# Kernel optimization log

Measured on AMD Instinct MI355X. Metric: run time of the kernel, lower is better.

Reference implementation:

```python
import jax, jax.numpy as jnp
import numpy as np

N_HEAD = 8
LINEAR_DIM = 64
IN_PIXELS = 4096  # h*w = 64*64
D = N_HEAD * LINEAR_DIM  # 512
C = 128
LN_EPS = 1e-6
BN_EPS = 1e-5


def setup_inputs() -> dict:
    key = jax.random.key(0)
    ks = jax.random.split(key, 10)
    shp = (16, C, 64, 64)
    # Kaiming-uniform-ish small init for weights (torch Linear weight layout: [out, in])
    def lin(k, out_f, in_f):
        lim = 1.0 / np.sqrt(in_f)
        return jax.random.uniform(k, (out_f, in_f), jnp.float32, -lim, lim)
    return {
        "v": jax.random.normal(ks[0], shp, jnp.float32),
        "k": jax.random.normal(ks[1], shp, jnp.float32),
        "q": jax.random.normal(ks[2], shp, jnp.float32),
        "w_qs": lin(ks[3], D, IN_PIXELS),
        "w_ks": lin(ks[4], D, IN_PIXELS),
        "w_vs": lin(ks[5], D, IN_PIXELS),
        "w_fc": lin(ks[6], IN_PIXELS, D),
        "ln_gamma": jnp.ones((D,), jnp.float32),
        "ln_beta": jnp.zeros((D,), jnp.float32),
        "temperature": jnp.asarray(IN_PIXELS ** 0.5, jnp.float32),
        "bn_gamma": jnp.ones((C,), jnp.float32),
        "bn_beta": jnp.zeros((C,), jnp.float32),
    }


def _layer_norm(x, gamma, beta):
    # torch-faithful: unbiased std (ddof=1), divide by (std + eps)
    mean = jnp.mean(x, axis=-1, keepdims=True)
    var = jnp.var(x, axis=-1, keepdims=True, ddof=1)
    std = jnp.sqrt(var)
    return gamma * (x - mean) / (std + LN_EPS) + beta


def reference(v, k, q, w_qs, w_ks, w_vs, w_fc, ln_gamma, ln_beta, temperature, bn_gamma, bn_beta):
    b, c, h, w = q.shape
    P = h * w
    qf = q.reshape(b, c, P)
    kf = k.reshape(b, c, P)
    vf = v.reshape(b, c, P)
    residual = vf
    # QKV projections: [b,c,P] @ W^T -> [b,c,D] -> [b,nh,c,ld]
    def proj(x, W):
        y = jnp.einsum('bcp,dp->bcd', x, W)
        return y.reshape(b, c, N_HEAD, LINEAR_DIM).transpose(0, 2, 1, 3)
    Q = proj(qf, w_qs)
    K = proj(kf, w_ks)
    V = proj(vf, w_vs)
    # channel-wise attention: scores [b,nh,c,c]
    scores = jnp.einsum('bhcd,bhed->bhce', Q / temperature, K)
    attn = jax.nn.softmax(scores, axis=-1)
    O = jnp.einsum('bhce,bhed->bhcd', attn, V)
    O = O.transpose(0, 2, 1, 3).reshape(b, c, N_HEAD * LINEAR_DIM)
    # Swish -> LayerNorm -> fc -> residual
    O = O * jax.nn.sigmoid(O)
    O = _layer_norm(O, ln_gamma, ln_beta)
    O = jnp.einsum('bcd,pd->bcp', O, w_fc)
    out = (residual + O).reshape(b, c, h, w)
    # BatchNorm2d in training mode: batch stats over (b,h,w), biased variance
    mean = jnp.mean(out, axis=(0, 2, 3), keepdims=True)
    var = jnp.var(out, axis=(0, 2, 3), keepdims=True)
    out = (out - mean) / jnp.sqrt(var + BN_EPS)
    out = out * bn_gamma[None, :, None, None] + bn_beta[None, :, None, None]
    return out
```

## Files before the change

### kernel.cpp

```cpp
#include <hip/hip_runtime.h>
#include <hip/hip_bf16.h>
#include <stdint.h>

typedef __attribute__((ext_vector_type(8))) short bf16x8;
typedef __attribute__((ext_vector_type(4))) float f32x4;

#define AS1(p) ((const __attribute__((address_space(1))) uint32_t*)(p))
#define AS3(p) ((__attribute__((address_space(3))) uint32_t*)(p))

__device__ __forceinline__ ushort f2bf(float f) {
  uint32_t u = __float_as_uint(f);
  uint32_t r = (u + 0x7fffu + ((u >> 16) & 1u)) >> 16;
  return (ushort)r;
}

__device__ __forceinline__ float bf2f(ushort u) {
  uint32_t v = ((uint32_t)u) << 16;
  return __uint_as_float(v);
}

__device__ __forceinline__ uint4 cvt8u(float4 a0, float4 a1) {
  uint4 r;
  asm("v_cvt_pk_bf16_f32 %0, %1, %2" : "=v"(r.x) : "v"(a0.x), "v"(a0.y));
  asm("v_cvt_pk_bf16_f32 %0, %1, %2" : "=v"(r.y) : "v"(a0.z), "v"(a0.w));
  asm("v_cvt_pk_bf16_f32 %0, %1, %2" : "=v"(r.z) : "v"(a1.x), "v"(a1.y));
  asm("v_cvt_pk_bf16_f32 %0, %1, %2" : "=v"(r.w) : "v"(a1.z), "v"(a1.w));
  return r;
}

__global__ __launch_bounds__(256) void pack4(
    const float* __restrict__ s0, const float* __restrict__ s1,
    const float* __restrict__ s2, const float* __restrict__ s3,
    ushort* __restrict__ o0, ushort* __restrict__ o1,
    ushort* __restrict__ o2, ushort* __restrict__ o3, int n)
{
  const float* s; ushort* o;
  switch (blockIdx.y) {
    case 0: s = s0; o = o0; break;
    case 1: s = s1; o = o1; break;
    case 2: s = s2; o = o2; break;
    default: s = s3; o = o3; break;
  }
  int stride = gridDim.x * 1024;
  for (int i = (blockIdx.x * 256 + threadIdx.x) * 4; i < n; i += stride) {
    float4 v = *(const float4*)(s + i);
    ushort4 u;
    u.x = f2bf(v.x); u.y = f2bf(v.y); u.z = f2bf(v.z); u.w = f2bf(v.w);
    *(ushort4*)(o + i) = u;
  }
}

__global__ __launch_bounds__(256) void gemm_qkv(
    const float* __restrict__ aq, const float* __restrict__ ak, const float* __restrict__ av,
    const ushort* __restrict__ wq, const ushort* __restrict__ wk, const ushort* __restrict__ wv,
    ushort* __restrict__ part, int lgs)
{
  __shared__ __align__(16) ushort At[128 * 64];
  __shared__ __align__(16) ushort Bt[2][128 * 64];
  int per = gridDim.x >> 3;
  int bid = blockIdx.x;
  int swz = (bid & 7) * per + (bid >> 3);
  int y = swz & 3, x = (swz >> 2) & 15, zz = swz >> 6;
  int g = zz >> lgs, s = zz & ((1 << lgs) - 1);
  const float* A; const ushort* Bm;
  if (g == 0)      { A = aq; Bm = wq; }
  else if (g == 1) { A = ak; Bm = wk; }
  else             { A = av; Bm = wv; }
  ushort* Pd = part + ((size_t)zz) * 1048576;
  const int K = 4096;
  const int kchunk = K >> lgs;
  const int k0 = s * kchunk, kend = k0 + kchunk;
  int rowBase = x * 128;
  int colBase = y * 128;
  int tid = threadIdx.x, l = tid & 63, w = tid >> 6;
  int wr = w >> 1, wc = w & 1, fr = l & 15, fq = l >> 4;

  int arow = tid >> 3;
  int aslot = tid & 7;
  const float* Abase = A + (size_t)(rowBase + arow) * K + aslot * 8;

  f32x4 acc[4][4];
#pragma unroll
  for (int m = 0; m < 4; ++m)
#pragma unroll
    for (int n = 0; n < 4; ++n) acc[m][n] = (f32x4){0.f, 0.f, 0.f, 0.f};

  float4 areg[4][2];
  auto loadA = [&](int ktn) {
#pragma unroll
    for (int j = 0; j < 4; ++j) {
      const float* p = Abase + (size_t)(j * 32) * K + ktn;
      areg[j][0] = *(const float4*)p;
      areg[j][1] = *(const float4*)(p + 4);
    }
  };
  auto cvtWriteA = [&]() {
#pragma unroll
    for (int j = 0; j < 4; ++j) {
      int row = j * 32 + arow;
      int sw = aslot ^ (row & 7);
      *(uint4*)((char*)At + row * 128 + sw * 16) = cvt8u(areg[j][0], areg[j][1]);
    }
  };
  auto stageB = [&](ushort* Bbuf, int ktn) {
#pragma unroll
    for (int j = 0; j < 4; ++j) {
      int c = ((w * 4 + j) << 6) + l;
      int row = c >> 3, slot = c & 7;
      int srccol = (slot ^ (row & 7)) * 8;
      __builtin_amdgcn_global_load_lds(AS1(Bm + (size_t)(colBase + row) * K + ktn + srccol),
                                       AS3((char*)Bbuf + c * 16), 16, 0, 0);
    }
  };
  auto mfmaPhase = [&](const ushort* Bbuf) {
#pragma unroll
    for (int kc = 0; kc < 2; ++kc) {
      bf16x8 af[4], bv[4];
#pragma unroll
      for (int m = 0; m < 4; ++m) {
        int r = wr * 64 + m * 16 + fr;
        int sl = (kc * 4 + fq) ^ (fr & 7);
        af[m] = *(const bf16x8*)((const char*)At + r * 128 + sl * 16);
      }
#pragma unroll
      for (int n = 0; n < 4; ++n) {
        int r = wc * 64 + n * 16 + fr;
        int sl = (kc * 4 + fq) ^ (fr & 7);
        bv[n] = *(const bf16x8*)((const char*)Bbuf + r * 128 + sl * 16);
      }
#pragma unroll
      for (int m = 0; m < 4; ++m)
#pragma unroll
        for (int n = 0; n < 4; ++n)
          acc[m][n] = __builtin_amdgcn_mfma_f32_16x16x32_bf16(af[m], bv[n], acc[m][n], 0, 0, 0);
    }
  };

  loadA(k0);
  stageB(Bt[0], k0);
  cvtWriteA();
  __syncthreads();

  int buf = 0;
#pragma unroll 1
  for (int kt = k0; kt < kend; kt += 64) {
    bool more = (kt + 64) < kend;
    if (more) { loadA(kt + 64); stageB(Bt[buf ^ 1], kt + 64); }
    mfmaPhase(Bt[buf]);
    __syncthreads();
    if (more) cvtWriteA();
    __syncthreads();
    buf ^= 1;
  }

#pragma unroll
  for (int m = 0; m < 4; ++m)
#pragma unroll
    for (int n = 0; n < 4; ++n)
#pragma unroll
      for (int r = 0; r < 4; ++r) {
        int row = rowBase + wr * 64 + m * 16 + fq * 4 + r;
        int col = colBase + wc * 64 + n * 16 + fr;
        Pd[(size_t)row * 512 + col] = f2bf(acc[m][n][r]);
      }
}

__global__ __launch_bounds__(256) void reduce_qkv(
    const ushort* __restrict__ part, ushort* __restrict__ Qp, ushort* __restrict__ Kp,
    ushort* __restrict__ Vp, int lgs)
{
  int g = blockIdx.y;
  ushort* dst = g == 0 ? Qp : (g == 1 ? Kp : Vp);
  const ushort* p = part + (((size_t)g) << lgs) * 1048576;
  int i = (blockIdx.x * 256 + threadIdx.x) * 8;
  int splits = 1 << lgs;
  float accv[8];
  {
    bf16x8 v = *(const bf16x8*)(p + i);
#pragma unroll
    for (int j = 0; j < 8; ++j) accv[j] = bf2f((ushort)v[j]);
  }
  for (int s = 1; s < splits; ++s) {
    bf16x8 v = *(const bf16x8*)(p + (size_t)s * 1048576 + i);
#pragma unroll
    for (int j = 0; j < 8; ++j) accv[j] += bf2f((ushort)v[j]);
  }
  ushort u[8];
#pragma unroll
  for (int j = 0; j < 8; ++j) u[j] = f2bf(accv[j]);
  *(uint4*)(dst + i) = *(uint4*)u;
}

__global__ __launch_bounds__(256) void attn(
    const ushort* __restrict__ Qp, const ushort* __restrict__ Kp, const ushort* __restrict__ Vp,
    float* __restrict__ Obuf, const float* __restrict__ temp)
{
  __shared__ __align__(16) ushort Qs[64 * 64];
  __shared__ __align__(16) ushort Ks[128 * 64];
  __shared__ __align__(16) ushort Vt[64 * 128];
  __shared__ __align__(16) float  Sl[64 * 128];
  __shared__ __align__(16) ushort Pl[64 * 128];
  __shared__ float rsum[64];
  int bh = blockIdx.y, b = bh >> 3, h = bh & 7;
  int c0 = blockIdx.x * 64;
  int tid = threadIdx.x, l = tid & 63, w = tid >> 6;
  int wr = w >> 1, wc = w & 1, fr = l & 15, fq = l >> 4;
  float invT = 1.0f / temp[0];
  const size_t rowQ = (size_t)(b * 128 + c0);

#pragma unroll
  for (int j = 0; j < 2; ++j) {
    int c = ((w * 2 + j) << 6) + l, row = c >> 3, cc = c & 7;
    __builtin_amdgcn_global_load_lds(AS1(Qp + (rowQ + row) * 512 + h * 64 + cc * 8),
                                     AS3((char*)Qs + (w * 2 + j) * 1024), 16, 0, 0);
  }
#pragma unroll
  for (int j = 0; j < 4; ++j) {
    int c = ((w * 4 + j) << 6) + l, row = c >> 3, cc = c & 7;
    __builtin_amdgcn_global_load_lds(AS1(Kp + (size_t)(b * 128 + row) * 512 + h * 64 + cc * 8),
                                     AS3((char*)Ks + (w * 4 + j) * 1024), 16, 0, 0);
  }
#pragma unroll
  for (int t = 0; t < 4; ++t) {
    int ch = tid + t * 256, e = ch >> 3, d0 = (ch & 7) * 8;
    bf16x8 vv = *(const bf16x8*)(Vp + (size_t)(b * 128 + e) * 512 + h * 64 + d0);
#pragma unroll
    for (int j = 0; j < 8; ++j) Vt[(d0 + j) * 128 + e] = (ushort)vv[j];
  }
  __syncthreads();

  f32x4 sa[2][4];
#pragma unroll
  for (int m = 0; m < 2; ++m)
#pragma unroll
    for (int n = 0; n < 4; ++n) sa[m][n] = (f32x4){0.f, 0.f, 0.f, 0.f};
#pragma unroll
  for (int kc = 0; kc < 2; ++kc) {
    bf16x8 aQ[2], bK[4];
#pragma unroll
    for (int m = 0; m < 2; ++m)
      aQ[m] = *(const bf16x8*)&Qs[(wr * 32 + m * 16 + fr) * 64 + kc * 32 + fq * 8];
#pragma unroll
    for (int n = 0; n < 4; ++n)
      bK[n] = *(const bf16x8*)&Ks[(wc * 64 + n * 16 + fr) * 64 + kc * 32 + fq * 8];
#pragma unroll
    for (int m = 0; m < 2; ++m)
#pragma unroll
      for (int n = 0; n < 4; ++n)
        sa[m][n] = __builtin_amdgcn_mfma_f32_16x16x32_bf16(aQ[m], bK[n], sa[m][n], 0, 0, 0);
  }
#pragma unroll
  for (int m = 0; m < 2; ++m)
#pragma unroll
    for (int n = 0; n < 4; ++n)
#pragma unroll
      for (int r = 0; r < 4; ++r)
        Sl[(wr * 32 + m * 16 + fq * 4 + r) * 128 + wc * 64 + n * 16 + fr] = sa[m][n][r] * invT;
  __syncthreads();

  {
    int row = tid >> 2, qq = tid & 3;
    const float* srow = Sl + row * 128 + qq * 32;
    float4 va[8];
#pragma unroll
    for (int i = 0; i < 8; ++i) va[i] = *(const float4*)(srow + i * 4);
    float mx = -1e30f;
#pragma unroll
    for (int i = 0; i < 8; ++i)
      mx = fmaxf(mx, fmaxf(fmaxf(va[i].x, va[i].y), fmaxf(va[i].z, va[i].w)));
    mx = fmaxf(mx, __shfl_xor(mx, 1));
    mx = fmaxf(mx, __shfl_xor(mx, 2));
    float ssum = 0.f;
    ushort* prow = Pl + row * 128 + qq * 32;
#pragma unroll
    for (int i = 0; i < 8; ++i) {
      float e0 = __expf(va[i].x - mx), e1 = __expf(va[i].y - mx);
      float e2 = __expf(va[i].z - mx), e3 = __expf(va[i].w - mx);
      ssum += (e0 + e1) + (e2 + e3);
      ushort4 u; u.x = f2bf(e0); u.y = f2bf(e1); u.z = f2bf(e2); u.w = f2bf(e3);
      *(ushort4*)(prow + i * 4) = u;
    }
    ssum += __shfl_xor(ssum, 1);
    ssum += __shfl_xor(ssum, 2);
    if (qq == 0) rsum[row] = ssum;
  }
  __syncthreads();

  f32x4 oa[2][2];
#pragma unroll
  for (int m = 0; m < 2; ++m)
#pragma unroll
    for (int n = 0; n < 2; ++n) oa[m][n] = (f32x4){0.f, 0.f, 0.f, 0.f};
#pragma unroll
  for (int kc = 0; kc < 4; ++kc) {
    bf16x8 aP[2], bV[2];
#pragma unroll
    for (int m = 0; m < 2; ++m)
      aP[m] = *(const bf16x8*)&Pl[(wr * 32 + m * 16 + fr) * 128 + kc * 32 + fq * 8];
#pragma unroll
    for (int n = 0; n < 2; ++n)
      bV[n] = *(const bf16x8*)&Vt[(wc * 32 + n * 16 + fr) * 128 + kc * 32 + fq * 8];
#pragma unroll
    for (int m = 0; m < 2; ++m)
#pragma unroll
      for (int n = 0; n < 2; ++n)
        oa[m][n] = __builtin_amdgcn_mfma_f32_16x16x32_bf16(aP[m], bV[n], oa[m][n], 0, 0, 0);
  }
#pragma unroll
  for (int m = 0; m < 2; ++m)
#pragma unroll
    for (int n = 0; n < 2; ++n)
#pragma unroll
      for (int r = 0; r < 4; ++r) {
        int row = wr * 32 + m * 16 + fq * 4 + r, col = wc * 32 + n * 16 + fr;
        Obuf[(rowQ + row) * 512 + h * 64 + col] = oa[m][n][r] / rsum[row];
      }
}

__global__ __launch_bounds__(256) void swish_ln(
    const float* __restrict__ O, ushort* __restrict__ X,
    const float* __restrict__ gamma, const float* __restrict__ beta)
{
  int row = blockIdx.x * 4 + (threadIdx.x >> 6);
  int lane = threadIdx.x & 63;
  const float* x = O + (size_t)row * 512 + lane * 8;
  float4 va = *(const float4*)(x);
  float4 vb = *(const float4*)(x + 4);
  float y[8] = {va.x, va.y, va.z, va.w, vb.x, vb.y, vb.z, vb.w};
  float s = 0.f, sq = 0.f;
#pragma unroll
  for (int i = 0; i < 8; ++i) {
    y[i] = y[i] / (1.f + __expf(-y[i]));
    s += y[i]; sq += y[i] * y[i];
  }
#pragma unroll
  for (int o = 1; o < 64; o <<= 1) { s += __shfl_xor(s, o); sq += __shfl_xor(sq, o); }
  float mean = s * (1.f / 512.f);
  float var = (sq - s * mean) * (1.f / 511.f);
  float inv = 1.f / (sqrtf(var) + 1e-6f);
  const float4 g0 = *(const float4*)(gamma + lane * 8);
  const float4 g1 = *(const float4*)(gamma + lane * 8 + 4);
  const float4 b0 = *(const float4*)(beta + lane * 8);
  const float4 b1 = *(const float4*)(beta + lane * 8 + 4);
  float gg[8] = {g0.x, g0.y, g0.z, g0.w, g1.x, g1.y, g1.z, g1.w};
  float bb[8] = {b0.x, b0.y, b0.z, b0.w, b1.x, b1.y, b1.z, b1.w};
  ushort u[8];
#pragma unroll
  for (int i = 0; i < 8; ++i) u[i] = f2bf(gg[i] * (y[i] - mean) * inv + bb[i]);
  *(uint4*)(X + (size_t)row * 512 + lane * 8) = *(uint4*)u;
}

__global__ __launch_bounds__(256) void gemm_fc(
    const ushort* __restrict__ A, const ushort* __restrict__ Bm,
    const float* __restrict__ resid, float* __restrict__ out,
    float* __restrict__ bn_sum, float* __restrict__ bn_sq)
{
  __shared__ __align__(16) ushort At[128 * 64];
  __shared__ __align__(16) ushort Bt[128 * 64];
  __shared__ float csum[128], csq[128];
  const int K = 512;
  int rowBase = blockIdx.x * 128;
  int colBase = blockIdx.y * 128;
  int tid = threadIdx.x, l = tid & 63, w = tid >> 6;
  int wr = w >> 1, wc = w & 1, fr = l & 15, fq = l >> 4;
  if (tid < 128) { csum[tid] = 0.f; csq[tid] = 0.f; }
  f32x4 acc[4][4];
#pragma unroll
  for (int m = 0; m < 4; ++m)
#pragma unroll
    for (int n = 0; n < 4; ++n) acc[m][n] = (f32x4){0.f, 0.f, 0.f, 0.f};

  for (int kt = 0; kt < K; kt += 64) {
#pragma unroll
    for (int j = 0; j < 4; ++j) {
      int c = ((w * 4 + j) << 6) + l;
      int row = c >> 3, cc = c & 7;
      __builtin_amdgcn_global_load_lds(AS1(A + (size_t)(rowBase + row) * K + kt + cc * 8),
                                       AS3((char*)At + (w * 4 + j) * 1024), 16, 0, 0);
      __builtin_amdgcn_global_load_lds(AS1(Bm + (size_t)(colBase + row) * K + kt + cc * 8),
                                       AS3((char*)Bt + (w * 4 + j) * 1024), 16, 0, 0);
    }
    __syncthreads();
#pragma unroll
    for (int kc = 0; kc < 2; ++kc) {
      bf16x8 af[4], bfv[4];
#pragma unroll
      for (int m = 0; m < 4; ++m)
        af[m] = *(const bf16x8*)&At[(wr * 64 + m * 16 + fr) * 64 + kc * 32 + fq * 8];
#pragma unroll
      for (int n = 0; n < 4; ++n)
        bfv[n] = *(const bf16x8*)&Bt[(wc * 64 + n * 16 + fr) * 64 + kc * 32 + fq * 8];
#pragma unroll
      for (int m = 0; m < 4; ++m)
#pragma unroll
        for (int n = 0; n < 4; ++n)
          acc[m][n] = __builtin_amdgcn_mfma_f32_16x16x32_bf16(af[m], bfv[n], acc[m][n], 0, 0, 0);
    }
    __syncthreads();
  }
#pragma unroll
  for (int m = 0; m < 4; ++m)
#pragma unroll
    for (int r = 0; r < 4; ++r) {
      float ps = 0.f, pq = 0.f;
#pragma unroll
      for (int n = 0; n < 4; ++n) {
        int row = rowBase + wr * 64 + m * 16 + fq * 4 + r;
        int col = colBase + wc * 64 + n * 16 + fr;
        size_t idx = (size_t)row * 4096 + col;
        float val = acc[m][n][r] + resid[idx];
        out[idx] = val;
        ps += val; pq += val * val;
      }
#pragma unroll
      for (int o = 1; o < 16; o <<= 1) { ps += __shfl_xor(ps, o); pq += __shfl_xor(pq, o); }
      if (fr == 0) {
        int ch = wr * 64 + m * 16 + fq * 4 + r;
        atomicAdd(&csum[ch], ps);
        atomicAdd(&csq[ch], pq);
      }
    }
  __syncthreads();
  if (tid < 128) {
    atomicAdd(&bn_sum[tid], csum[tid]);
    atomicAdd(&bn_sq[tid], csq[tid]);
  }
}

__global__ __launch_bounds__(256) void bn_norm(
    float* __restrict__ out, const float* __restrict__ bn_sum, const float* __restrict__ bn_sq,
    const float* __restrict__ gamma, const float* __restrict__ beta)
{
  __shared__ float sc[128], sh[128];
  const float inv_n = 1.f / 65536.f;
  int tid = threadIdx.x;
  if (tid < 128) {
    float mean = bn_sum[tid] * inv_n;
    float var = bn_sq[tid] * inv_n - mean * mean;
    float g = gamma[tid] * rsqrtf(var + 1e-5f);
    sc[tid] = g;
    sh[tid] = beta[tid] - mean * g;
  }
  __syncthreads();
  int stride = gridDim.x * blockDim.x;
  for (int v = blockIdx.x * blockDim.x + tid; v < 2097152; v += stride) {
    int elem = v * 4;
    int ch = (elem >> 12) & 127;
    float g = sc[ch], bta = sh[ch];
    float4 x = *(float4*)(out + elem);
    x.x = x.x * g + bta;
    x.y = x.y * g + bta;
    x.z = x.z * g + bta;
    x.w = x.w * g + bta;
    *(float4*)(out + elem) = x;
  }
}

extern "C" void kernel_launch(void* const* d_in, const int* in_sizes, int n_in,
                              void* d_out, int out_size, void* d_ws, size_t ws_size,
                              hipStream_t stream)
{
  const float* v_in = (const float*)d_in[0];
  const float* k_in = (const float*)d_in[1];
  const float* q_in = (const float*)d_in[2];
  const float* w_qs = (const float*)d_in[3];
  const float* w_ks = (const float*)d_in[4];
  const float* w_vs = (const float*)d_in[5];
  const float* w_fc = (const float*)d_in[6];
  const float* ln_g = (const float*)d_in[7];
  const float* ln_b = (const float*)d_in[8];
  const float* temp = (const float*)d_in[9];
  const float* bn_g = (const float*)d_in[10];
  const float* bn_b = (const float*)d_in[11];
  float* out = (float*)d_out;

  char* ws = (char*)d_ws;
  size_t off = 0;
  auto alloc = [&](size_t bytes) { char* p = ws + off; off += bytes; return p; };
  ushort* wq  = (ushort*)alloc(512ull * 4096 * 2);
  ushort* wk  = (ushort*)alloc(512ull * 4096 * 2);
  ushort* wv  = (ushort*)alloc(512ull * 4096 * 2);
  ushort* wfc = (ushort*)alloc(512ull * 4096 * 2);
  ushort* Qp  = (ushort*)alloc(2048ull * 512 * 2);
  ushort* Kp  = (ushort*)alloc(2048ull * 512 * 2);
  ushort* Vp  = (ushort*)alloc(2048ull * 512 * 2);
  float*  Obuf= (float*)alloc(2048ull * 512 * 4);
  ushort* X16 = (ushort*)alloc(2048ull * 512 * 2);
  float*  bns = (float*)alloc(128 * 4);
  float*  bnq = (float*)alloc(128 * 4);

  int lgs = 2;
  if (off + (3ull << lgs) * 1048576 * 2 > ws_size) lgs = 1;
  if (off + (3ull << lgs) * 1048576 * 2 > ws_size) lgs = 0;
  ushort* part = (ushort*)alloc((3ull << lgs) * 1048576 * 2);

  hipMemsetAsync(bns, 0, 256 * 4, stream);

  pack4<<<dim3(512, 4), 256, 0, stream>>>(w_qs, w_ks, w_vs, w_fc, wq, wk, wv, wfc,
                                          512 * 4096);
  gemm_qkv<<<16 * 4 * (3 << lgs), 256, 0, stream>>>(q_in, k_in, v_in, wq, wk, wv, part, lgs);
  reduce_qkv<<<dim3(512, 3), 256, 0, stream>>>(part, Qp, Kp, Vp, lgs);
  attn<<<dim3(2, 128), 256, 0, stream>>>(Qp, Kp, Vp, Obuf, temp);
  swish_ln<<<512, 256, 0, stream>>>(Obuf, X16, ln_g, ln_b);
  gemm_fc<<<dim3(16, 32), 256, 0, stream>>>(X16, wfc, v_in, out, bns, bnq);
  bn_norm<<<2048, 256, 0, stream>>>(out, bns, bnq, bn_g, bn_b);
}
```

Baseline: 116.0 us.

## Hand-schedule QKV GEMM waits and store pre-BN values as bf16

The QKV GEMM main loop is rewritten with explicit vmcnt/lgkmcnt waits, raw s_barrier and sched_barrier in place of two __syncthreads per iteration, and it adds a 3-blocks-per-CU launch bound to overlap global loads with MFMA. Separately, gemm_fc now writes the pre-BatchNorm values to a bf16 scratch buffer, and bn_norm reads that buffer and writes fp32 output. This cuts intermediate memory traffic. The risk is precision loss from rounding the pre-normalisation values to bf16 before the final output, and fragile manual wait counts.

```diff
diff --git a/kernel.cpp b/kernel.cpp
--- a/kernel.cpp
+++ b/kernel.cpp
@@ -7,6 +7,12 @@
 
 #define AS1(p) ((const __attribute__((address_space(1))) uint32_t*)(p))
 #define AS3(p) ((__attribute__((address_space(3))) uint32_t*)(p))
+
+#define VM12   asm volatile("s_waitcnt vmcnt(12)")
+#define VM0    asm volatile("s_waitcnt vmcnt(0)")
+#define LG0    asm volatile("s_waitcnt lgkmcnt(0)")
+#define SBAR   __builtin_amdgcn_s_barrier()
+#define SCHED0 __builtin_amdgcn_sched_barrier(0)
 
 __device__ __forceinline__ ushort f2bf(float f) {
   uint32_t u = __float_as_uint(f);
@@ -50,7 +56,7 @@
   }
 }
 
-__global__ __launch_bounds__(256) void gemm_qkv(
+__global__ __launch_bounds__(256, 3) void gemm_qkv(
     const float* __restrict__ aq, const float* __restrict__ ak, const float* __restrict__ av,
     const ushort* __restrict__ wq, const ushort* __restrict__ wk, const ushort* __restrict__ wv,
     ushort* __restrict__ part, int lgs)
@@ -77,7 +83,9 @@
 
   int arow = tid >> 3;
   int aslot = tid & 7;
+  int aswz = aslot ^ (arow & 7);
   const float* Abase = A + (size_t)(rowBase + arow) * K + aslot * 8;
+  char* At0 = (char*)At + arow * 128 + aswz * 16;
 
   f32x4 acc[4][4];
 #pragma unroll
@@ -85,73 +93,93 @@
 #pragma unroll
     for (int n = 0; n < 4; ++n) acc[m][n] = (f32x4){0.f, 0.f, 0.f, 0.f};
 
-  float4 areg[4][2];
-  auto loadA = [&](int ktn) {
-#pragma unroll
-    for (int j = 0; j < 4; ++j) {
-      const float* p = Abase + (size_t)(j * 32) * K + ktn;
-      areg[j][0] = *(const float4*)p;
-      areg[j][1] = *(const float4*)(p + 4);
-    }
-  };
-  auto cvtWriteA = [&]() {
-#pragma unroll
-    for (int j = 0; j < 4; ++j) {
-      int row = j * 32 + arow;
-      int sw = aslot ^ (row & 7);
-      *(uint4*)((char*)At + row * 128 + sw * 16) = cvt8u(areg[j][0], areg[j][1]);
-    }
-  };
-  auto stageB = [&](ushort* Bbuf, int ktn) {
-#pragma unroll
-    for (int j = 0; j < 4; ++j) {
-      int c = ((w * 4 + j) << 6) + l;
-      int row = c >> 3, slot = c & 7;
-      int srccol = (slot ^ (row & 7)) * 8;
-      __builtin_amdgcn_global_load_lds(AS1(Bm + (size_t)(colBase + row) * K + ktn + srccol),
-                                       AS3((char*)Bbuf + c * 16), 16, 0, 0);
-    }
-  };
-  auto mfmaPhase = [&](const ushort* Bbuf) {
-#pragma unroll
-    for (int kc = 0; kc < 2; ++kc) {
-      bf16x8 af[4], bv[4];
-#pragma unroll
-      for (int m = 0; m < 4; ++m) {
-        int r = wr * 64 + m * 16 + fr;
-        int sl = (kc * 4 + fq) ^ (fr & 7);
-        af[m] = *(const bf16x8*)((const char*)At + r * 128 + sl * 16);
-      }
-#pragma unroll
-      for (int n = 0; n < 4; ++n) {
-        int r = wc * 64 + n * 16 + fr;
-        int sl = (kc * 4 + fq) ^ (fr & 7);
-        bv[n] = *(const bf16x8*)((const char*)Bbuf + r * 128 + sl * 16);
-      }
-#pragma unroll
-      for (int m = 0; m < 4; ++m)
-#pragma unroll
-        for (int n = 0; n < 4; ++n)
-          acc[m][n] = __builtin_amdgcn_mfma_f32_16x16x32_bf16(af[m], bv[n], acc[m][n], 0, 0, 0);
-    }
-  };
-
-  loadA(k0);
-  stageB(Bt[0], k0);
-  cvtWriteA();
-  __syncthreads();
+  float4 a0, a1, a2, a3, a4, a5, a6, a7;
+
+#define LOADA(ktn) do { \
+    a0 = *(const float4*)(Abase + (size_t)0 * K + (ktn)); \
+    a1 = *(const float4*)(Abase + (size_t)0 * K + (ktn) + 4); \
+    a2 = *(const float4*)(Abase + (size_t)32 * K + (ktn)); \
+    a3 = *(const float4*)(Abase + (size_t)32 * K + (ktn) + 4); \
+    a4 = *(const float4*)(Abase + (size_t)64 * K + (ktn)); \
+    a5 = *(const float4*)(Abase + (size_t)64 * K + (ktn) + 4); \
+    a6 = *(const float4*)(Abase + (size_t)96 * K + (ktn)); \
+    a7 = *(const float4*)(Abase + (size_t)96 * K + (ktn) + 4); \
+  } while (0)
+
+#define CVTWRITEA do { \
+    *(uint4*)(At0 + 0 * 4096)  = cvt8u(a0, a1); \
+    *(uint4*)(At0 + 1 * 4096)  = cvt8u(a2, a3); \
+    *(uint4*)(At0 + 2 * 4096)  = cvt8u(a4, a5); \
+    *(uint4*)(At0 + 3 * 4096)  = cvt8u(a6, a7); \
+  } while (0)
+
+#define STAGEB(bufIdx, ktn) do { \
+    char* Bbuf_ = (char*)Bt[bufIdx]; \
+    _Pragma("unroll") \
+    for (int j = 0; j < 4; ++j) { \
+      int c = ((w * 4 + j) << 6) + l; \
+      int row = c >> 3, slot = c & 7; \
+      int srccol = (slot ^ (row & 7)) * 8; \
+      __builtin_amdgcn_global_load_lds(AS1(Bm + (size_t)(colBase + row) * K + (ktn) + srccol), \
+                                       AS3(Bbuf_ + c * 16), 16, 0, 0); \
+    } \
+  } while (0)
+
+#define MFMAPHASE(bufIdx) do { \
+    const char* Bbuf_ = (const char*)Bt[bufIdx]; \
+    _Pragma("unroll") \
+    for (int kc = 0; kc < 2; ++kc) { \
+      bf16x8 af[4], bv[4]; \
+      _Pragma("unroll") \
+      for (int m = 0; m < 4; ++m) { \
+        int r = wr * 64 + m * 16 + fr; \
+        int sl = (kc * 4 + fq) ^ (fr & 7); \
+        af[m] = *(const bf16x8*)((const char*)At + r * 128 + sl * 16); \
+      } \
+      _Pragma("unroll") \
+      for (int n = 0; n < 4; ++n) { \
+        int r = wc * 64 + n * 16 + fr; \
+        int sl = (kc * 4 + fq) ^ (fr & 7); \
+        bv[n] = *(const bf16x8*)(Bbuf_ + r * 128 + sl * 16); \
+      } \
+      _Pragma("unroll") \
+      for (int m = 0; m < 4; ++m) \
+        _Pragma("unroll") \
+        for (int n = 0; n < 4; ++n) \
+          acc[m][n] = __builtin_amdgcn_mfma_f32_16x16x32_bf16(af[m], bv[n], acc[m][n], 0, 0, 0); \
+    } \
+  } while (0)
+
+  LOADA(k0);
+  STAGEB(0, k0);
+  CVTWRITEA;
+  LG0; SCHED0;
 
   int buf = 0;
 #pragma unroll 1
   for (int kt = k0; kt < kend; kt += 64) {
     bool more = (kt + 64) < kend;
-    if (more) { loadA(kt + 64); stageB(Bt[buf ^ 1], kt + 64); }
-    mfmaPhase(Bt[buf]);
-    __syncthreads();
-    if (more) cvtWriteA();
-    __syncthreads();
+    if (more) {
+      LOADA(kt + 64);
+      STAGEB(buf ^ 1, kt + 64);
+      VM12; SCHED0;
+    } else {
+      VM0; SCHED0;
+    }
+    SBAR; SCHED0;
+    MFMAPHASE(buf);
+    SBAR;
+    if (more) {
+      CVTWRITEA;
+      LG0; SCHED0;
+    }
     buf ^= 1;
   }
+
+#undef LOADA
+#undef CVTWRITEA
+#undef STAGEB
+#undef MFMAPHASE
 
 #pragma unroll
   for (int m = 0; m < 4; ++m)
@@ -352,7 +380,7 @@
 
 __global__ __launch_bounds__(256) void gemm_fc(
     const ushort* __restrict__ A, const ushort* __restrict__ Bm,
-    const float* __restrict__ resid, float* __restrict__ out,
+    const float* __restrict__ resid, ushort* __restrict__ valb,
     float* __restrict__ bn_sum, float* __restrict__ bn_sq)
 {
   __shared__ __align__(16) ushort At[128 * 64];
@@ -409,7 +437,7 @@
         int col = colBase + wc * 64 + n * 16 + fr;
         size_t idx = (size_t)row * 4096 + col;
         float val = acc[m][n][r] + resid[idx];
-        out[idx] = val;
+        valb[idx] = f2bf(val);
         ps += val; pq += val * val;
       }
 #pragma unroll
@@ -428,7 +456,8 @@
 }
 
 __global__ __launch_bounds__(256) void bn_norm(
-    float* __restrict__ out, const float* __restrict__ bn_sum, const float* __restrict__ bn_sq,
+    const ushort* __restrict__ valb, float* __restrict__ out,
+    const float* __restrict__ bn_sum, const float* __restrict__ bn_sq,
     const float* __restrict__ gamma, const float* __restrict__ beta)
 {
   __shared__ float sc[128], sh[128];
@@ -443,16 +472,22 @@
   }
   __syncthreads();
   int stride = gridDim.x * blockDim.x;
-  for (int v = blockIdx.x * blockDim.x + tid; v < 2097152; v += stride) {
-    int elem = v * 4;
+  for (int v = blockIdx.x * blockDim.x + tid; v < 1048576; v += stride) {
+    int elem = v * 8;
     int ch = (elem >> 12) & 127;
     float g = sc[ch], bta = sh[ch];
-    float4 x = *(float4*)(out + elem);
-    x.x = x.x * g + bta;
-    x.y = x.y * g + bta;
-    x.z = x.z * g + bta;
-    x.w = x.w * g + bta;
-    *(float4*)(out + elem) = x;
+    bf16x8 x = *(const bf16x8*)(valb + elem);
+    float4 o0, o1;
+    o0.x = bf2f((ushort)x[0]) * g + bta;
+    o0.y = bf2f((ushort)x[1]) * g + bta;
+    o0.z = bf2f((ushort)x[2]) * g + bta;
+    o0.w = bf2f((ushort)x[3]) * g + bta;
+    o1.x = bf2f((ushort)x[4]) * g + bta;
+    o1.y = bf2f((ushort)x[5]) * g + bta;
+    o1.z = bf2f((ushort)x[6]) * g + bta;
+    o1.w = bf2f((ushort)x[7]) * g + bta;
+    *(float4*)(out + elem) = o0;
+    *(float4*)(out + elem + 4) = o1;
   }
 }
 
@@ -486,6 +521,7 @@
   ushort* Vp  = (ushort*)alloc(2048ull * 512 * 2);
   float*  Obuf= (float*)alloc(2048ull * 512 * 4);
   ushort* X16 = (ushort*)alloc(2048ull * 512 * 2);
+  ushort* valb= (ushort*)alloc(2048ull * 4096 * 2);
   float*  bns = (float*)alloc(128 * 4);
   float*  bnq = (float*)alloc(128 * 4);
 
@@ -502,6 +538,6 @@
   reduce_qkv<<<dim3(512, 3), 256, 0, stream>>>(part, Qp, Kp, Vp, lgs);
   attn<<<dim3(2, 128), 256, 0, stream>>>(Qp, Kp, Vp, Obuf, temp);
   swish_ln<<<512, 256, 0, stream>>>(Obuf, X16, ln_g, ln_b);
-  gemm_fc<<<dim3(16, 32), 256, 0, stream>>>(X16, wfc, v_in, out, bns, bnq);
-  bn_norm<<<2048, 256, 0, stream>>>(out, bns, bnq, bn_g, bn_b);
-}
+  gemm_fc<<<dim3(16, 32), 256, 0, stream>>>(X16, wfc, v_in, valb, bns, bnq);
+  bn_norm<<<2048, 256, 0, stream>>>(valb, out, bns, bnq, bn_g, bn_b);
+}
```

New measurement: 114.8 us. Within noise of the previous version (-1.1%).
